# Optimization experiments

Hardware: AMD Instinct MI355X
Metric: run time of the kernel (lower is better)

Reference implementation:

```python
import jax, jax.numpy as jnp
import numpy as np

EPS = 1e-8


def setup_inputs() -> dict:
    key = jax.random.key(0)
    ks = jax.random.split(key, 7)
    S, B, E, D, A = 2048, 32, 1024, 1024, 1024
    return {
        "decoder_state": jax.random.normal(ks[0], (B, D), jnp.float32),
        "encoder_states": jax.random.normal(ks[1], (S, B, E), jnp.float32),
        "noise": jax.random.normal(ks[2], (S, B), jnp.float32),
        "W_dec": jax.random.normal(ks[3], (D, A), jnp.float32) * (D ** -0.5),
        "W_enc": jax.random.normal(ks[4], (E, A), jnp.float32) * (E ** -0.5),
        "b": jax.random.normal(ks[5], (A,), jnp.float32) * 0.02,
        "v": jax.random.normal(ks[6], (A,), jnp.float32) * (A ** -0.5),
    }


def reference(decoder_state, encoder_states, noise, W_dec, W_enc, b, v):
    S, B, E = encoder_states.shape
    # Additive (Bahdanau) monotonic energy: e_sb = v . tanh(W_d s + W_e h + b)
    dec_proj = decoder_state @ W_dec                         # [B, A]
    enc_proj = jnp.einsum("sbe,ea->sba", encoder_states, W_enc)  # [S, B, A]
    energy = jnp.einsum("sba,a->sb", jnp.tanh(enc_proj + dec_proj[None] + b), v)
    # p_choose with pre-sigmoid Gaussian noise (noise_avg=0, noise_var=1)
    p_choose = jax.nn.sigmoid(energy + noise)                # [S, B]

    # previous_attention is None -> one-hot at source position 0
    prev_attn = jnp.zeros((S, B), p_choose.dtype).at[0].set(1.0)

    # exclusive cumprod of (1 - p) along src dim
    cp = jnp.cumprod(1.0 - p_choose, axis=0)
    cumprod_one_minus_p = jnp.concatenate(
        [jnp.ones((1, B), p_choose.dtype), cp[:-1]], axis=0)
    denom = jnp.clip(cumprod_one_minus_p, EPS, 1.0)
    alpha = p_choose * cumprod_one_minus_p * jnp.cumsum(prev_attn / denom, axis=0)

    # mass preservation (no padding mask): dump residual mass on last frame
    residual = 1.0 - jnp.clip(jnp.sum(alpha[:-1], axis=0), 0.0, 1.0)
    alpha = alpha.at[-1].set(residual)

    beta = alpha  # hard monotonic attention: beta == alpha
    weighted_context = jnp.einsum("sbe,sb->be", encoder_states, beta)  # [B, E]
    return weighted_context, alpha
```

## Files before the change

### kernel.cpp

```cpp
#include <hip/hip_runtime.h>
#include <hip/hip_fp16.h>

#define S_DIM 2048
#define B_DIM 32
#define E_DIM 1024
#define A_DIM 1024
#define D_DIM 1024
#define M_DIM (S_DIM * B_DIM)

typedef _Float16 f16x8 __attribute__((ext_vector_type(8)));
typedef _Float16 f16x4 __attribute__((ext_vector_type(4)));
typedef float f32x4 __attribute__((ext_vector_type(4)));

#define OFF_ENC 0ull
#define OFF_WT  134217728ull
#define OFF_DP  (OFF_WT + 2097152ull)
#define OFF_EN  (OFF_DP + 131072ull)

__device__ inline void load_lds16(const void* g, void* l) {
    __builtin_amdgcn_global_load_lds((const __attribute__((address_space(1))) void*)g,
                                     (__attribute__((address_space(3))) void*)l, 16, 0, 0);
}

__global__ void convert_enc_kernel(const float4* __restrict__ in, f16x4* __restrict__ out) {
    int idx = blockIdx.x * 256 + threadIdx.x;
    float4 f = in[idx];
    f16x4 o = { (_Float16)f.x, (_Float16)f.y, (_Float16)f.z, (_Float16)f.w };
    out[idx] = o;
}

__global__ void transpose_wenc_kernel(const float* __restrict__ W, _Float16* __restrict__ WT) {
    __shared__ _Float16 tile[32][33];
    int a0 = blockIdx.x * 32, e0 = blockIdx.y * 32;
    int tx = threadIdx.x & 31, ty = threadIdx.x >> 5;
    #pragma unroll
    for (int i = 0; i < 32; i += 8)
        tile[ty + i][tx] = (_Float16)W[(size_t)(e0 + ty + i) * A_DIM + a0 + tx];
    __syncthreads();
    #pragma unroll
    for (int i = 0; i < 32; i += 8)
        WT[(size_t)(a0 + ty + i) * E_DIM + e0 + tx] = tile[tx][ty + i];
}

__global__ void decproj_kernel(const float* __restrict__ dec, const float* __restrict__ Wd,
                               const float* __restrict__ bias, float* __restrict__ dp) {
    const int t = threadIdx.x;
    const int a = blockIdx.x * 64 + (t & 63);
    const int bg = t >> 6;
    const int d0 = blockIdx.y * 256;
    float acc[8] = {};
    #pragma unroll 4
    for (int d = d0; d < d0 + 256; ++d) {
        float w = Wd[(size_t)d * A_DIM + a];
        #pragma unroll
        for (int bi = 0; bi < 8; ++bi)
            acc[bi] += dec[(size_t)(bg * 8 + bi) * D_DIM + d] * w;
    }
    #pragma unroll
    for (int bi = 0; bi < 8; ++bi) {
        float add = acc[bi] + (blockIdx.y == 0 ? bias[a] : 0.f);
        atomicAdd(&dp[(size_t)(bg * 8 + bi) * A_DIM + a], add);
    }
}

__global__ __launch_bounds__(512, 2)
void energy_gemm_kernel(const _Float16* __restrict__ Af, const _Float16* __restrict__ Bt,
                        const float* __restrict__ dp, const float* __restrict__ v,
                        float* __restrict__ energy) {
    __shared__ alignas(16) _Float16 As[4][256 * 32];
    __shared__ alignas(16) _Float16 Bs[4][256 * 32];

    const int tid = threadIdx.x;
    const int wid = tid >> 6;
    const int lane = tid & 63;
    const int quad = lane >> 4;
    const int l15 = lane & 15;
    const int rsw = ((l15 >> 1) & 3);

    const int bid = blockIdx.x;
    const int xcd = bid & 7;
    const int local = bid >> 3;
    const int m0 = (xcd * 32 + (local >> 2)) * 256;
    const int n0 = (local & 3) * 256;

    const int wm = (wid >> 2) * 128;
    const int wn = (wid & 3) * 64;

    const int lr = lane >> 2;
    const int lc = ((lane & 3) ^ ((lane >> 3) & 3)) * 8;
    const _Float16* Ag = Af + (size_t)(m0 + wid * 16 + lr) * E_DIM + lc;
    const _Float16* Bg = Bt + (size_t)(n0 + wid * 16 + lr) * E_DIM + lc;

#define STAGE_A(u)                                                              \
    {                                                                           \
        load_lds16(Ag + (size_t)(u) * 32, &As[(u) & 3][wid * 512]);             \
        load_lds16(Ag + (size_t)128 * E_DIM + (size_t)(u) * 32,                 \
                   &As[(u) & 3][(wid + 8) * 512]);                              \
    }
#define STAGE_B(u)                                                              \
    {                                                                           \
        load_lds16(Bg + (size_t)(u) * 32, &Bs[(u) & 3][wid * 512]);             \
        load_lds16(Bg + (size_t)128 * E_DIM + (size_t)(u) * 32,                 \
                   &Bs[(u) & 3][(wid + 8) * 512]);                              \
    }

    f32x4 acc[8][4] = {};

    STAGE_A(0) STAGE_B(0)
    STAGE_A(1) STAGE_B(1)
    STAGE_A(2) STAGE_B(2)
    asm volatile("s_waitcnt vmcnt(8)" ::: "memory");
    __builtin_amdgcn_s_barrier();
    asm volatile("" ::: "memory");

    #pragma unroll
    for (int t = 0; t < 32; ++t) {
        const int slot = t & 3;
        f16x8 af[4], bf[4];

        #pragma unroll
        for (int j = 0; j < 4; ++j)
            bf[j] = *(const f16x8*)&Bs[slot][(wn + j * 16 + l15) * 32 + (quad ^ rsw) * 8];
        #pragma unroll
        for (int i = 0; i < 4; ++i)
            af[i] = *(const f16x8*)&As[slot][(wm + i * 16 + l15) * 32 + (quad ^ rsw) * 8];
        if (t < 29) STAGE_A(t + 3)
        asm volatile("" ::: "memory");
        __builtin_amdgcn_s_barrier();
        asm volatile("" ::: "memory");
        __builtin_amdgcn_s_setprio(1);
        #pragma unroll
        for (int i = 0; i < 4; ++i)
            #pragma unroll
            for (int j = 0; j < 4; ++j)
                acc[i][j] = __builtin_amdgcn_mfma_f32_16x16x32_f16(af[i], bf[j], acc[i][j], 0, 0, 0);
        __builtin_amdgcn_s_setprio(0);
        asm volatile("" ::: "memory");
        __builtin_amdgcn_s_barrier();
        asm volatile("" ::: "memory");

        #pragma unroll
        for (int i = 0; i < 4; ++i)
            af[i] = *(const f16x8*)&As[slot][(wm + 64 + i * 16 + l15) * 32 + (quad ^ rsw) * 8];
        if (t < 29) STAGE_B(t + 3)
        asm volatile("" ::: "memory");
        __builtin_amdgcn_s_barrier();
        asm volatile("" ::: "memory");
        __builtin_amdgcn_s_setprio(1);
        #pragma unroll
        for (int i = 0; i < 4; ++i)
            #pragma unroll
            for (int j = 0; j < 4; ++j)
                acc[4 + i][j] = __builtin_amdgcn_mfma_f32_16x16x32_f16(af[i], bf[j], acc[4 + i][j], 0, 0, 0);
        __builtin_amdgcn_s_setprio(0);
        if (t <= 28)      asm volatile("s_waitcnt vmcnt(8)" ::: "memory");
        else if (t == 29) asm volatile("s_waitcnt vmcnt(4)" ::: "memory");
        else if (t == 30) asm volatile("s_waitcnt vmcnt(0)" ::: "memory");
        asm volatile("" ::: "memory");
        __builtin_amdgcn_s_barrier();
        asm volatile("" ::: "memory");
    }
#undef STAGE_A
#undef STAGE_B

    float vf[4];
    #pragma unroll
    for (int j = 0; j < 4; ++j) vf[j] = v[n0 + wn + j * 16 + l15];

    #pragma unroll
    for (int i = 0; i < 8; ++i) {
        #pragma unroll
        for (int r = 0; r < 4; ++r) {
            int m = m0 + wm + i * 16 + quad * 4 + r;
            int bidx = m & 31;
            float sum = 0.f;
            #pragma unroll
            for (int j = 0; j < 4; ++j) {
                int a = n0 + wn + j * 16 + l15;
                float x = acc[i][j][r] + dp[bidx * A_DIM + a];
                float ex = __expf(2.f * x);
                float th = 1.f - 2.f * __builtin_amdgcn_rcpf(ex + 1.f);
                sum += th * vf[j];
            }
            sum += __shfl_xor(sum, 1);
            sum += __shfl_xor(sum, 2);
            sum += __shfl_xor(sum, 4);
            sum += __shfl_xor(sum, 8);
            if (l15 == 0) atomicAdd(&energy[bidx * S_DIM + (m >> 5)], sum);
        }
    }
}

__global__ void scan_alpha_kernel(const float* __restrict__ energy, const float* __restrict__ noise,
                                  float* __restrict__ alpha) {
    __shared__ float sc[256];
    __shared__ float red[256];
    const int b = blockIdx.x;
    const int t = threadIdx.x;
    float p[8], q[8];
    float prod = 1.f;
    #pragma unroll
    for (int k = 0; k < 8; ++k) {
        int s = t * 8 + k;
        float x = energy[b * S_DIM + s] + noise[s * B_DIM + b];
        p[k] = __builtin_amdgcn_rcpf(1.f + __expf(-x));
        q[k] = __builtin_amdgcn_rcpf(1.f + __expf(x));
        prod *= q[k];
    }
    sc[t] = prod;
    __syncthreads();
    for (int off = 1; off < 256; off <<= 1) {
        float mine = sc[t];
        float other = (t >= off) ? sc[t - off] : 1.f;
        __syncthreads();
        sc[t] = mine * other;
        __syncthreads();
    }
    float run = (t > 0) ? sc[t - 1] : 1.f;
    float lsum = 0.f;
    #pragma unroll
    for (int k = 0; k < 8; ++k) {
        int s = t * 8 + k;
        float al = p[k] * run;
        run *= q[k];
        if (s < S_DIM - 1) { alpha[s * B_DIM + b] = al; lsum += al; }
    }
    red[t] = lsum;
    __syncthreads();
    for (int off = 128; off > 0; off >>= 1) {
        if (t < off) red[t] += red[t + off];
        __syncthreads();
    }
    if (t == 0) {
        float tot = fminf(fmaxf(red[0], 0.f), 1.f);
        alpha[(S_DIM - 1) * B_DIM + b] = 1.f - tot;
    }
}

__global__ void wc_kernel(const _Float16* __restrict__ enc, const float* __restrict__ alpha,
                          float* __restrict__ wc) {
    __shared__ float red[128][8];
    const int b = blockIdx.y;
    const int t = threadIdx.x;
    const int e0 = (t & 127) * 8;
    const int half = t >> 7;
    int s = blockIdx.x * 128 + half;
    float acc[8] = {};
    for (int i = 0; i < 64; ++i, s += 2) {
        float al = alpha[s * B_DIM + b];
        f16x8 r = *(const f16x8*)&enc[((size_t)s * B_DIM + b) * E_DIM + e0];
        #pragma unroll
        for (int k = 0; k < 8; ++k) acc[k] += al * (float)r[k];
    }
    if (half) {
        #pragma unroll
        for (int k = 0; k < 8; ++k) red[t - 128][k] = acc[k];
    }
    __syncthreads();
    if (!half) {
        #pragma unroll
        for (int k = 0; k < 8; ++k)
            atomicAdd(&wc[b * E_DIM + e0 + k], acc[k] + red[t][k]);
    }
}

extern "C" void kernel_launch(void* const* d_in, const int* in_sizes, int n_in,
                              void* d_out, int out_size, void* d_ws, size_t ws_size,
                              hipStream_t stream) {
    const float* dec   = (const float*)d_in[0];
    const float* enc   = (const float*)d_in[1];
    const float* noise = (const float*)d_in[2];
    const float* Wd    = (const float*)d_in[3];
    const float* We    = (const float*)d_in[4];
    const float* bias  = (const float*)d_in[5];
    const float* v     = (const float*)d_in[6];

    char* ws = (char*)d_ws;
    _Float16* encf = (_Float16*)(ws + OFF_ENC);
    _Float16* wtf  = (_Float16*)(ws + OFF_WT);
    float* dp      = (float*)(ws + OFF_DP);
    float* energy  = (float*)(ws + OFF_EN);

    float* wc    = (float*)d_out;
    float* alpha = (float*)d_out + B_DIM * E_DIM;

    (void)hipMemsetAsync(wc, 0, B_DIM * E_DIM * sizeof(float), stream);
    (void)hipMemsetAsync(dp, 0, B_DIM * A_DIM * sizeof(float), stream);
    (void)hipMemsetAsync(energy, 0, M_DIM * sizeof(float), stream);

    convert_enc_kernel<<<dim3(M_DIM * E_DIM / 4 / 256), 256, 0, stream>>>((const float4*)enc, (f16x4*)encf);
    transpose_wenc_kernel<<<dim3(32, 32), 256, 0, stream>>>(We, wtf);
    decproj_kernel<<<dim3(16, 4), 256, 0, stream>>>(dec, Wd, bias, dp);
    energy_gemm_kernel<<<dim3(1024), 512, 0, stream>>>(encf, wtf, dp, v, energy);
    scan_alpha_kernel<<<dim3(32), 256, 0, stream>>>(energy, noise, alpha);
    wc_kernel<<<dim3(16, 32), 256, 0, stream>>>(encf, alpha, wc);
}
```

Baseline: 640.1 us.

## Double-buffer MFMA fragments in registers and cut barriers to one per k-step

The GEMM main loop now loads A and B fragments for the next k-tile from LDS into a second register set while MFMAs run on the current set. This replaces the old scheme, which split each k-step into two half-tiles and used four barriers per step. Both global-to-LDS stages for step t+3 are issued together, and vmcnt waits are adjusted so one barrier per step suffices. The goal is to hide LDS read latency and cut synchronisation stalls. The cost is roughly 24 extra f16x8 fragment registers, which could raise VGPR pressure and lower occupancy.

Measured after the change: 634.4 us. About the same (-0.9%).

```diff
diff --git a/kernel.cpp b/kernel.cpp
--- a/kernel.cpp
+++ b/kernel.cpp
@@ -105,61 +105,55 @@
     }
 
     f32x4 acc[8][4] = {};
+    f16x8 afA[8], bfA[4], afB[8], bfB[4];
 
     STAGE_A(0) STAGE_B(0)
     STAGE_A(1) STAGE_B(1)
     STAGE_A(2) STAGE_B(2)
-    asm volatile("s_waitcnt vmcnt(8)" ::: "memory");
+    asm volatile("s_waitcnt vmcnt(4)" ::: "memory");
     __builtin_amdgcn_s_barrier();
     asm volatile("" ::: "memory");
 
     #pragma unroll
-    for (int t = 0; t < 32; ++t) {
-        const int slot = t & 3;
-        f16x8 af[4], bf[4];
-
-        #pragma unroll
-        for (int j = 0; j < 4; ++j)
-            bf[j] = *(const f16x8*)&Bs[slot][(wn + j * 16 + l15) * 32 + (quad ^ rsw) * 8];
-        #pragma unroll
-        for (int i = 0; i < 4; ++i)
-            af[i] = *(const f16x8*)&As[slot][(wm + i * 16 + l15) * 32 + (quad ^ rsw) * 8];
-        if (t < 29) STAGE_A(t + 3)
-        asm volatile("" ::: "memory");
-        __builtin_amdgcn_s_barrier();
-        asm volatile("" ::: "memory");
-        __builtin_amdgcn_s_setprio(1);
-        #pragma unroll
-        for (int i = 0; i < 4; ++i)
-            #pragma unroll
-            for (int j = 0; j < 4; ++j)
-                acc[i][j] = __builtin_amdgcn_mfma_f32_16x16x32_f16(af[i], bf[j], acc[i][j], 0, 0, 0);
-        __builtin_amdgcn_s_setprio(0);
-        asm volatile("" ::: "memory");
-        __builtin_amdgcn_s_barrier();
-        asm volatile("" ::: "memory");
-
-        #pragma unroll
-        for (int i = 0; i < 4; ++i)
-            af[i] = *(const f16x8*)&As[slot][(wm + 64 + i * 16 + l15) * 32 + (quad ^ rsw) * 8];
-        if (t < 29) STAGE_B(t + 3)
-        asm volatile("" ::: "memory");
-        __builtin_amdgcn_s_barrier();
-        asm volatile("" ::: "memory");
-        __builtin_amdgcn_s_setprio(1);
-        #pragma unroll
-        for (int i = 0; i < 4; ++i)
-            #pragma unroll
-            for (int j = 0; j < 4; ++j)
-                acc[4 + i][j] = __builtin_amdgcn_mfma_f32_16x16x32_f16(af[i], bf[j], acc[4 + i][j], 0, 0, 0);
-        __builtin_amdgcn_s_setprio(0);
-        if (t <= 28)      asm volatile("s_waitcnt vmcnt(8)" ::: "memory");
-        else if (t == 29) asm volatile("s_waitcnt vmcnt(4)" ::: "memory");
-        else if (t == 30) asm volatile("s_waitcnt vmcnt(0)" ::: "memory");
-        asm volatile("" ::: "memory");
-        __builtin_amdgcn_s_barrier();
-        asm volatile("" ::: "memory");
-    }
+    for (int j = 0; j < 4; ++j)
+        bfA[j] = *(const f16x8*)&Bs[0][(wn + j * 16 + l15) * 32 + (quad ^ rsw) * 8];
+    #pragma unroll
+    for (int i = 0; i < 8; ++i)
+        afA[i] = *(const f16x8*)&As[0][(wm + i * 16 + l15) * 32 + (quad ^ rsw) * 8];
+
+#define TILE(t, afC, bfC, afN, bfN)                                             \
+    {                                                                           \
+        if ((t) <= 28) { STAGE_A((t) + 3) STAGE_B((t) + 3) }                    \
+        __builtin_amdgcn_s_setprio(1);                                          \
+        _Pragma("unroll")                                                       \
+        for (int i = 0; i < 8; ++i) {                                           \
+            if ((t) < 31 && i < 4)                                              \
+                bfN[i] = *(const f16x8*)&Bs[((t) + 1) & 3]                      \
+                    [(wn + i * 16 + l15) * 32 + (quad ^ rsw) * 8];              \
+            if ((t) < 31)                                                       \
+                afN[i] = *(const f16x8*)&As[((t) + 1) & 3]                      \
+                    [(wm + i * 16 + l15) * 32 + (quad ^ rsw) * 8];              \
+            _Pragma("unroll")                                                   \
+            for (int j = 0; j < 4; ++j)                                         \
+                acc[i][j] = __builtin_amdgcn_mfma_f32_16x16x32_f16(             \
+                    afC[i], bfC[j], acc[i][j], 0, 0, 0);                        \
+        }                                                                       \
+        __builtin_amdgcn_s_setprio(0);                                          \
+        if ((t) <= 28)      asm volatile("s_waitcnt vmcnt(4)" ::: "memory");    \
+        else if ((t) == 29) asm volatile("s_waitcnt vmcnt(0)" ::: "memory");    \
+        if ((t) < 31) {                                                         \
+            asm volatile("" ::: "memory");                                      \
+            __builtin_amdgcn_s_barrier();                                       \
+            asm volatile("" ::: "memory");                                      \
+        }                                                                       \
+    }
+
+    #pragma unroll
+    for (int tt = 0; tt < 32; tt += 2) {
+        TILE(tt,     afA, bfA, afB, bfB)
+        TILE(tt + 1, afB, bfB, afA, bfA)
+    }
+#undef TILE
 #undef STAGE_A
 #undef STAGE_B
 
```
